# Kernel tuning notes

Measured on AMD Instinct MI355X. Metric: run time of the kernel, lower is better.

## Reference

```python
import jax, jax.numpy as jnp
import numpy as np

N_HEADS = 8
PROJ_DIM = 32


def _phi(x):
    # elu(x) + 1 feature map (always > 0)
    return jax.nn.elu(x) + 1.0


def _causal_linear(pq, pk, v):
    # Faithful to torch _linear_kernelized_attention masked branch:
    #   dpq_l = pq_l - pq_{l-1} (with pq_{-1}=0)
    #   result_l = cumsum_{m<=l} (dpq_m . v_m) * pk_m
    # The torch code materializes (N,H,L,D,D); here the identical math is
    # computed via a per-position scalar c_m = dpq_m . v_m, O(L*D) memory.
    dpq = pq - jnp.concatenate([jnp.zeros_like(pq[..., :1, :]), pq[..., :-1, :]], axis=-2)
    c = jnp.einsum('nhld,nhld->nhl', dpq, v)[..., None]  # (N,H,L,1)
    return jnp.cumsum(c * pk, axis=-2)  # (N,H,L,D)


def _bidir_linear(pq, pk, v):
    # Non-masked linear path: (pk^T v) first, then pq @ (.)
    right = jnp.einsum('nhld,nhle->nhde', pk, v)
    return jnp.einsum('nhqd,nhde->nhqe', pq, right)


def _attention(Y, X, Wq, Wk, Wv, mask):
    N, Lq, Dm = Y.shape
    Lk = X.shape[1]
    H, Pd = N_HEADS, PROJ_DIM
    # torch Linear: x @ W^T
    q = (Y @ Wq.T).reshape(N, Lq, H, Pd).transpose(0, 2, 1, 3)  # (N,H,Lq,Pd)
    k = (X @ Wk.T).reshape(N, Lk, H, Pd).transpose(0, 2, 1, 3)
    v = (X @ Wv.T).reshape(N, Lk, H, Pd).transpose(0, 2, 1, 3)
    pq, pk = _phi(q), _phi(k)
    fn = _causal_linear if mask else _bidir_linear
    num = fn(pq, pk, v)
    den = fn(pq, pk, jnp.ones_like(v))  # v_scale = ones expanded to D
    A = num / den
    return A.transpose(0, 2, 1, 3).reshape(N, Lq, H * Pd)


def setup_inputs() -> dict:
    key = jax.random.key(0)
    kY, kX, kq, kk, kv = jax.random.split(key, 5)
    N, L, dim = 2, 8192, N_HEADS * PROJ_DIM
    scale_in = 0.05            # keep phi(q),phi(k) ~ 1 so denominator stays positive
    scale_w = 1.0 / np.sqrt(dim)
    Y = scale_in * jax.random.normal(kY, (N, L, dim), dtype=jnp.float32)
    X = scale_in * jax.random.normal(kX, (N, L, dim), dtype=jnp.float32)
    Wq = scale_w * jax.random.normal(kq, (dim, dim), dtype=jnp.float32)
    Wk = scale_w * jax.random.normal(kk, (dim, dim), dtype=jnp.float32)
    Wv = scale_w * jax.random.normal(kv, (dim, dim), dtype=jnp.float32)
    return {"Y": Y, "X": X, "Wq": Wq, "Wk": Wk, "Wv": Wv, "mask": 1}


def reference(Y, X, Wq, Wk, Wv, mask):
    return _attention(Y, X, Wq, Wk, Wv, mask)
```

## Files before the change

kernel.cpp:

```cpp
#include <hip/hip_runtime.h>
#include <hip/hip_bf16.h>


typedef __attribute__((ext_vector_type(8))) short short8;
typedef __attribute__((ext_vector_type(4))) float f32x4;

__device__ __forceinline__ float phi_f(float x) {
    return x > 0.f ? x + 1.f : __expf(x);
}
__device__ __forceinline__ unsigned short f2bf(float x) {
    __hip_bfloat16 h = __float2bfloat16(x);
    return *reinterpret_cast<unsigned short*>(&h);
}
__device__ __forceinline__ float bf2f(unsigned short u) {
    return __uint_as_float(((unsigned int)u) << 16);
}

__global__ __launch_bounds__(256) void k_prepw(
        const float* __restrict__ Wq, const float* __restrict__ Wk,
        const float* __restrict__ Wv, unsigned short* __restrict__ Wf)
{
    const int g = blockIdx.x * 256 + threadIdx.x;
    const int mat = g >> 13, cc = g & 8191;
    const float* src = (mat == 0) ? Wq : (mat == 1 ? Wv : Wk);
    const int ln = cc & 15, qd = (cc >> 4) & 3, kt = (cc >> 6) & 7, jt = cc >> 9;
    const float* s = src + (size_t)(jt * 16 + ln) * 256 + kt * 32 + qd * 8;
    f32x4 f0 = __builtin_nontemporal_load((const f32x4*)s);
    f32x4 f1 = __builtin_nontemporal_load((const f32x4*)(s + 4));
    short8 o;
    o[0] = f2bf(f0[0]); o[1] = f2bf(f0[1]); o[2] = f2bf(f0[2]); o[3] = f2bf(f0[3]);
    o[4] = f2bf(f1[0]); o[5] = f2bf(f1[1]); o[6] = f2bf(f1[2]); o[7] = f2bf(f1[3]);
    *(short8*)(Wf + (size_t)g * 8) = o;
}

#define LDA 280

__global__ __launch_bounds__(512, 4) void k_gemm(
        const float* __restrict__ Y, const float* __restrict__ X,
        const unsigned short* __restrict__ Wf,
        unsigned short* __restrict__ pk_out,
        float* __restrict__ c_out, float* __restrict__ cd_out,
        float* __restrict__ tot)
{
    __shared__ __align__(16) unsigned short Ys[33 * LDA];
    __shared__ __align__(16) unsigned short Xs[32 * LDA];
    __shared__ float scc[32][8], scd[32][8];
    __shared__ __align__(16) unsigned short spk[32 * 264];

    const int rb = blockIdx.x;
    const int n = rb >> 8, tile = rb & 255;
    const int mbase = rb * 32, lseg0 = tile * 32;
    const bool hasprev = (tile != 0);
    const int t = threadIdx.x, w = t >> 6, lane = t & 63;
    const int ln = lane & 15, qd = lane >> 4;

#pragma unroll
    for (int it = 0; it < 8; ++it) {
        const int idx = t + it * 512;
        const int half = idx >> 11, row = (idx >> 6) & 31, c4 = idx & 63;
        const float* s = (half ? X : Y) + (size_t)(mbase + row) * 256 + c4 * 4;
        f32x4 f = __builtin_nontemporal_load((const f32x4*)s);
        ushort4 h4;
        h4.x = f2bf(f[0]); h4.y = f2bf(f[1]); h4.z = f2bf(f[2]); h4.w = f2bf(f[3]);
        unsigned short* dst = half ? Xs : Ys;
        *(ushort4*)&dst[row * LDA + c4 * 4] = h4;
    }
    if (t < 64) {
        const int prow = hasprev ? mbase - 1 : mbase;
        f32x4 f = __builtin_nontemporal_load((const f32x4*)(Y + (size_t)prow * 256 + t * 4));
        ushort4 h4;
        h4.x = f2bf(f[0]); h4.y = f2bf(f[1]); h4.z = f2bf(f[2]); h4.w = f2bf(f[3]);
        *(ushort4*)&Ys[32 * LDA + t * 4] = h4;
    }
    __syncthreads();

    f32x4 aq[2][2], av[2][2], akk[2][2], aqp[2];
#pragma unroll
    for (int i = 0; i < 2; ++i)
#pragma unroll
        for (int j = 0; j < 2; ++j) {
            aq[i][j]  = (f32x4){0.f, 0.f, 0.f, 0.f};
            av[i][j]  = (f32x4){0.f, 0.f, 0.f, 0.f};
            akk[i][j] = (f32x4){0.f, 0.f, 0.f, 0.f};
        }
    aqp[0] = (f32x4){0.f, 0.f, 0.f, 0.f};
    aqp[1] = (f32x4){0.f, 0.f, 0.f, 0.f};
    const short8 z8 = {0, 0, 0, 0, 0, 0, 0, 0};
    const short8* W8 = (const short8*)Wf;

#pragma unroll
    for (int kt = 0; kt < 8; ++kt) {
        const int ko = kt * 32 + qd * 8;
        short8 ay0 = *(const short8*)&Ys[ln * LDA + ko];
        short8 ay1 = *(const short8*)&Ys[(16 + ln) * LDA + ko];
        short8 ax0 = *(const short8*)&Xs[ln * LDA + ko];
        short8 ax1 = *(const short8*)&Xs[(16 + ln) * LDA + ko];
        short8 ext = *(const short8*)&Ys[32 * LDA + ko];
        short8 ayp = (ln == 15) ? ext : z8;
#pragma unroll
        for (int jj = 0; jj < 2; ++jj) {
            const int jt = w * 2 + jj;
            short8 bq = W8[(((0 * 16 + jt) * 8 + kt) << 6) + lane];
            short8 bv = W8[(((1 * 16 + jt) * 8 + kt) << 6) + lane];
            short8 bk = W8[(((2 * 16 + jt) * 8 + kt) << 6) + lane];
            aq[0][jj]  = __builtin_amdgcn_mfma_f32_16x16x32_bf16(ay0, bq, aq[0][jj], 0, 0, 0);
            aq[1][jj]  = __builtin_amdgcn_mfma_f32_16x16x32_bf16(ay1, bq, aq[1][jj], 0, 0, 0);
            aqp[jj]    = __builtin_amdgcn_mfma_f32_16x16x32_bf16(ayp, bq, aqp[jj], 0, 0, 0);
            av[0][jj]  = __builtin_amdgcn_mfma_f32_16x16x32_bf16(ax0, bv, av[0][jj], 0, 0, 0);
            av[1][jj]  = __builtin_amdgcn_mfma_f32_16x16x32_bf16(ax1, bv, av[1][jj], 0, 0, 0);
            akk[0][jj] = __builtin_amdgcn_mfma_f32_16x16x32_bf16(ax0, bk, akk[0][jj], 0, 0, 0);
            akk[1][jj] = __builtin_amdgcn_mfma_f32_16x16x32_bf16(ax1, bk, akk[1][jj], 0, 0, 0);
        }
    }

#pragma unroll
    for (int i = 0; i < 2; ++i)
#pragma unroll
        for (int jj = 0; jj < 2; ++jj)
#pragma unroll
            for (int r = 0; r < 4; ++r) aq[i][jj][r] = phi_f(aq[i][jj][r]);
    float pprev[2];
#pragma unroll
    for (int jj = 0; jj < 2; ++jj) {
        float p15 = __shfl(aqp[jj][3], 48 + ln);
        pprev[jj] = hasprev ? phi_f(p15) : 0.f;
    }

    float cc_[2][4], cd_[2][4];
#pragma unroll
    for (int i = 0; i < 2; ++i)
#pragma unroll
        for (int r = 0; r < 4; ++r) { cc_[i][r] = 0.f; cd_[i][r] = 0.f; }
#pragma unroll
    for (int jj = 0; jj < 2; ++jj) {
        float carry = pprev[jj];
#pragma unroll
        for (int i = 0; i < 2; ++i) {
            const float p0 = aq[i][jj][0], p1 = aq[i][jj][1], p2 = aq[i][jj][2], p3 = aq[i][jj][3];
            const float up3 = __shfl_up(p3, 16);
            const float prev0 = (qd == 0) ? carry : up3;
            const float d0 = p0 - prev0, d1 = p1 - p0, d2 = p2 - p1, d3 = p3 - p2;
            cc_[i][0] += d0 * av[i][jj][0]; cd_[i][0] += d0;
            cc_[i][1] += d1 * av[i][jj][1]; cd_[i][1] += d1;
            cc_[i][2] += d2 * av[i][jj][2]; cd_[i][2] += d2;
            cc_[i][3] += d3 * av[i][jj][3]; cd_[i][3] += d3;
            carry = __shfl(p3, ln + 48);
        }
    }
#pragma unroll
    for (int i = 0; i < 2; ++i)
#pragma unroll
        for (int r = 0; r < 4; ++r) {
            float x = cc_[i][r];
            x += __shfl_xor(x, 1); x += __shfl_xor(x, 2);
            x += __shfl_xor(x, 4); x += __shfl_xor(x, 8);
            float y = cd_[i][r];
            y += __shfl_xor(y, 1); y += __shfl_xor(y, 2);
            y += __shfl_xor(y, 4); y += __shfl_xor(y, 8);
            if (ln == 0) {
                scc[i * 16 + qd * 4 + r][w] = x;
                scd[i * 16 + qd * 4 + r][w] = y;
            }
        }
    __syncthreads();
    {
        const int idx = t & 255, row = idx & 31, h = idx >> 5;
        const size_t gi = (size_t)(n * 8 + h) * 8192 + lseg0 + row;
        if (t < 256) __builtin_nontemporal_store(scc[row][h], &c_out[gi]);
        else         __builtin_nontemporal_store(scd[row][h], &cd_out[gi]);
    }

#pragma unroll
    for (int i = 0; i < 2; ++i)
#pragma unroll
        for (int jj = 0; jj < 2; ++jj)
#pragma unroll
            for (int r = 0; r < 4; ++r) akk[i][jj][r] = phi_f(akk[i][jj][r]);
#pragma unroll
    for (int jj = 0; jj < 2; ++jj) {
        float tn = 0.f, td = 0.f;
#pragma unroll
        for (int i = 0; i < 2; ++i)
#pragma unroll
            for (int r = 0; r < 4; ++r) {
                const int row = i * 16 + qd * 4 + r;
                const float pv = akk[i][jj][r];
                tn += scc[row][w] * pv;
                td += scd[row][w] * pv;
            }
        tn += __shfl_xor(tn, 16); tn += __shfl_xor(tn, 32);
        td += __shfl_xor(td, 16); td += __shfl_xor(td, 32);
        if (qd == 0) {
            const int d = jj * 16 + ln;
            const size_t bi = ((size_t)(n * 8 + w) * 256 + tile) * 64;
            __builtin_nontemporal_store(tn, &tot[bi + d]);
            __builtin_nontemporal_store(td, &tot[bi + 32 + d]);
        }
    }

#pragma unroll
    for (int i = 0; i < 2; ++i)
#pragma unroll
        for (int jj = 0; jj < 2; ++jj)
#pragma unroll
            for (int r = 0; r < 4; ++r)
                spk[(i * 16 + qd * 4 + r) * 264 + w * 32 + jj * 16 + ln] = f2bf(akk[i][jj][r]);
    __syncthreads();
#pragma unroll
    for (int it = 0; it < 2; ++it) {
        const int idx = t + 512 * it;
        const int row = idx >> 5, cg = idx & 31;
        short8 vals = *(const short8*)&spk[row * 264 + cg * 8];
        const int head = cg >> 2, d8 = (cg & 3) * 8;
        __builtin_nontemporal_store(
            vals, (short8*)(pk_out + ((size_t)(n * 8 + head) * 8192 + lseg0 + row) * 32 + d8));
    }
}

__global__ __launch_bounds__(256) void k_scan(
        const unsigned short* __restrict__ pk, const float* __restrict__ c,
        const float* __restrict__ cd, const float* __restrict__ tot,
        float* __restrict__ out)
{
    __shared__ __align__(16) unsigned short spk[128 * 32];
    __shared__ float sc[128], sd[128];
    __shared__ float wsum[4][64], stile[4][64];

    const int bx = blockIdx.x, seg = bx >> 6, blk = bx & 63;
    const int n = seg >> 3, h = seg & 7;
    const int t = threadIdx.x, l0 = blk * 128;
    const int wv = t >> 6, lane = t & 63;
    const int T = blk * 4;

    const float* tb = tot + (size_t)seg * 256 * 64 + lane;
    float p0 = 0.f, p1 = 0.f, p2 = 0.f, p3 = 0.f,
          p4 = 0.f, p5 = 0.f, p6 = 0.f, p7 = 0.f;
    int i = wv;
    for (; i + 28 < T; i += 32) {
        p0 += tb[(i)      * 64]; p1 += tb[(i + 4)  * 64];
        p2 += tb[(i + 8)  * 64]; p3 += tb[(i + 12) * 64];
        p4 += tb[(i + 16) * 64]; p5 += tb[(i + 20) * 64];
        p6 += tb[(i + 24) * 64]; p7 += tb[(i + 28) * 64];
    }
    for (; i < T; i += 4) p0 += tb[i * 64];
    wsum[wv][lane]  = ((p0 + p1) + (p2 + p3)) + ((p4 + p5) + (p6 + p7));
    stile[wv][lane] = tb[(T + wv) * 64];

#pragma unroll
    for (int it = 0; it < 2; ++it) {
        const int idx = t + 256 * it;
        short8 vv = __builtin_nontemporal_load(
            (const short8*)(pk + ((size_t)seg * 8192 + l0) * 32 + idx * 8));
        *(short8*)&spk[idx * 8] = vv;
    }
    if (t < 128) sc[t] = __builtin_nontemporal_load(&c[(size_t)seg * 8192 + l0 + t]);
    else         sd[t - 128] = __builtin_nontemporal_load(&cd[(size_t)seg * 8192 + l0 + (t - 128)]);
    __syncthreads();

    if (t < 128) {
        const int g = t >> 5, d = t & 31;
        float rn  = (wsum[0][d] + wsum[1][d]) + (wsum[2][d] + wsum[3][d]);
        float rd_ = (wsum[0][32 + d] + wsum[1][32 + d]) + (wsum[2][32 + d] + wsum[3][32 + d]);
#pragma unroll
        for (int i2 = 0; i2 < 3; ++i2)
            if (i2 < g) { rn += stile[i2][d]; rd_ += stile[i2][32 + d]; }
        float* ob = out + ((size_t)n * 8192 + l0 + g * 32) * 256 + h * 32 + d;
#pragma unroll
        for (int p = 0; p < 32; ++p) {
            const int m = g * 32 + p;
            const float pkv = bf2f(spk[m * 32 + d]);
            rn  += sc[m] * pkv;
            rd_ += sd[m] * pkv;
            __builtin_nontemporal_store(rn / rd_, &ob[(size_t)p * 256]);
        }
    }
}

extern "C" void kernel_launch(void* const* d_in, const int* in_sizes, int n_in,
                              void* d_out, int out_size, void* d_ws, size_t ws_size,
                              hipStream_t stream)
{
    const float* Y  = (const float*)d_in[0];
    const float* X  = (const float*)d_in[1];
    const float* Wq = (const float*)d_in[2];
    const float* Wk = (const float*)d_in[3];
    const float* Wv = (const float*)d_in[4];
    float* out = (float*)d_out;

    float* ws = (float*)d_ws;
    unsigned short* Wf = (unsigned short*)ws;
    unsigned short* pk = (unsigned short*)(ws + 98304);
    float* c   = ws + 98304 + 2097152;
    float* cd  = c  + 131072;
    float* tot = cd + 131072;

    hipLaunchKernelGGL(k_prepw, dim3(96),   dim3(256), 0, stream, Wq, Wk, Wv, Wf);
    hipLaunchKernelGGL(k_gemm,  dim3(512),  dim3(512), 0, stream,
                       Y, X, Wf, pk, c, cd, tot);
    hipLaunchKernelGGL(k_scan,  dim3(1024), dim3(256), 0, stream, pk, c, cd, tot, out);
}
```

Measured before the change: 116.0 us.

## Process 64-row tiles per GEMM block with prefetched weight fragments and cached stores

Each k_gemm block now handles two 32-row tiles (64 rows), so every weight fragment loaded from global memory feeds twice as many MFMAs. The grid is halved to 256 blocks. The weight fragments are prefetched two k-steps ahead through a three-slot register ring. Nontemporal stores and loads for the pk, c, cd and tot intermediates become ordinary ones, so the scan kernel can hit them in cache. In exchange, register and LDS use roughly double and occupancy drops to 2 blocks per CU. With only 256 blocks, the GPU may also be underfilled.

```diff
diff --git a/kernel.cpp b/kernel.cpp
--- a/kernel.cpp
+++ b/kernel.cpp
@@ -35,29 +35,30 @@
 
 #define LDA 280
 
-__global__ __launch_bounds__(512, 4) void k_gemm(
+__global__ __launch_bounds__(512, 2) void k_gemm(
         const float* __restrict__ Y, const float* __restrict__ X,
         const unsigned short* __restrict__ Wf,
         unsigned short* __restrict__ pk_out,
         float* __restrict__ c_out, float* __restrict__ cd_out,
         float* __restrict__ tot)
 {
-    __shared__ __align__(16) unsigned short Ys[33 * LDA];
-    __shared__ __align__(16) unsigned short Xs[32 * LDA];
-    __shared__ float scc[32][8], scd[32][8];
-    __shared__ __align__(16) unsigned short spk[32 * 264];
+    __shared__ __align__(16) unsigned short Ys[65 * LDA];
+    __shared__ __align__(16) unsigned short Xs[64 * LDA];
+    __shared__ float scc[64][8], scd[64][8];
+    __shared__ __align__(16) unsigned short spk[64 * 264];
 
     const int rb = blockIdx.x;
-    const int n = rb >> 8, tile = rb & 255;
-    const int mbase = rb * 32, lseg0 = tile * 32;
-    const bool hasprev = (tile != 0);
+    const int n = rb >> 7, tpair = rb & 127;
+    const int mbase = rb * 64;
+    const int tile0 = tpair * 2, lseg0 = tpair * 64;
+    const bool hasprev = (tpair != 0);
     const int t = threadIdx.x, w = t >> 6, lane = t & 63;
     const int ln = lane & 15, qd = lane >> 4;
 
 #pragma unroll
-    for (int it = 0; it < 8; ++it) {
+    for (int it = 0; it < 16; ++it) {
         const int idx = t + it * 512;
-        const int half = idx >> 11, row = (idx >> 6) & 31, c4 = idx & 63;
+        const int half = idx >> 12, row = (idx >> 6) & 63, c4 = idx & 63;
         const float* s = (half ? X : Y) + (size_t)(mbase + row) * 256 + c4 * 4;
         f32x4 f = __builtin_nontemporal_load((const f32x4*)s);
         ushort4 h4;
@@ -70,55 +71,83 @@
         f32x4 f = __builtin_nontemporal_load((const f32x4*)(Y + (size_t)prow * 256 + t * 4));
         ushort4 h4;
         h4.x = f2bf(f[0]); h4.y = f2bf(f[1]); h4.z = f2bf(f[2]); h4.w = f2bf(f[3]);
-        *(ushort4*)&Ys[32 * LDA + t * 4] = h4;
+        *(ushort4*)&Ys[64 * LDA + t * 4] = h4;
     }
     __syncthreads();
 
-    f32x4 aq[2][2], av[2][2], akk[2][2], aqp[2];
-#pragma unroll
-    for (int i = 0; i < 2; ++i)
-#pragma unroll
-        for (int j = 0; j < 2; ++j) {
-            aq[i][j]  = (f32x4){0.f, 0.f, 0.f, 0.f};
-            av[i][j]  = (f32x4){0.f, 0.f, 0.f, 0.f};
-            akk[i][j] = (f32x4){0.f, 0.f, 0.f, 0.f};
-        }
+    f32x4 aq[2][2][2], av[2][2][2], akk[2][2][2], aqp[2];
+#pragma unroll
+    for (int t2 = 0; t2 < 2; ++t2)
+#pragma unroll
+        for (int i = 0; i < 2; ++i)
+#pragma unroll
+            for (int j = 0; j < 2; ++j) {
+                aq[t2][i][j]  = (f32x4){0.f, 0.f, 0.f, 0.f};
+                av[t2][i][j]  = (f32x4){0.f, 0.f, 0.f, 0.f};
+                akk[t2][i][j] = (f32x4){0.f, 0.f, 0.f, 0.f};
+            }
     aqp[0] = (f32x4){0.f, 0.f, 0.f, 0.f};
     aqp[1] = (f32x4){0.f, 0.f, 0.f, 0.f};
     const short8 z8 = {0, 0, 0, 0, 0, 0, 0, 0};
     const short8* W8 = (const short8*)Wf;
+    const int jt0 = 2 * w;
+
+    short8 Bq[3][2], Bv[3][2], Bk[3][2];
+#define LOADB(slot, kt_)                                                   \
+    {                                                                      \
+        _Pragma("unroll")                                                  \
+        for (int jj = 0; jj < 2; ++jj) {                                   \
+            const int jt = jt0 + jj;                                       \
+            Bq[slot][jj] = W8[(((0 * 16 + jt) * 8 + (kt_)) << 6) + lane];  \
+            Bv[slot][jj] = W8[(((1 * 16 + jt) * 8 + (kt_)) << 6) + lane];  \
+            Bk[slot][jj] = W8[(((2 * 16 + jt) * 8 + (kt_)) << 6) + lane];  \
+        }                                                                  \
+    }
+    LOADB(0, 0);
+    LOADB(1, 1);
 
 #pragma unroll
     for (int kt = 0; kt < 8; ++kt) {
+        if (kt + 2 < 8) LOADB((kt + 2) % 3, kt + 2);
         const int ko = kt * 32 + qd * 8;
-        short8 ay0 = *(const short8*)&Ys[ln * LDA + ko];
-        short8 ay1 = *(const short8*)&Ys[(16 + ln) * LDA + ko];
-        short8 ax0 = *(const short8*)&Xs[ln * LDA + ko];
-        short8 ax1 = *(const short8*)&Xs[(16 + ln) * LDA + ko];
-        short8 ext = *(const short8*)&Ys[32 * LDA + ko];
+        short8 ay[2][2], ax[2][2];
+#pragma unroll
+        for (int t2 = 0; t2 < 2; ++t2)
+#pragma unroll
+            for (int i = 0; i < 2; ++i) {
+                ay[t2][i] = *(const short8*)&Ys[(t2 * 32 + i * 16 + ln) * LDA + ko];
+                ax[t2][i] = *(const short8*)&Xs[(t2 * 32 + i * 16 + ln) * LDA + ko];
+            }
+        short8 ext = *(const short8*)&Ys[64 * LDA + ko];
         short8 ayp = (ln == 15) ? ext : z8;
+        const int sl = kt % 3;
 #pragma unroll
         for (int jj = 0; jj < 2; ++jj) {
-            const int jt = w * 2 + jj;
-            short8 bq = W8[(((0 * 16 + jt) * 8 + kt) << 6) + lane];
-            short8 bv = W8[(((1 * 16 + jt) * 8 + kt) << 6) + lane];
-            short8 bk = W8[(((2 * 16 + jt) * 8 + kt) << 6) + lane];
-            aq[0][jj]  = __builtin_amdgcn_mfma_f32_16x16x32_bf16(ay0, bq, aq[0][jj], 0, 0, 0);
-            aq[1][jj]  = __builtin_amdgcn_mfma_f32_16x16x32_bf16(ay1, bq, aq[1][jj], 0, 0, 0);
-            aqp[jj]    = __builtin_amdgcn_mfma_f32_16x16x32_bf16(ayp, bq, aqp[jj], 0, 0, 0);
-            av[0][jj]  = __builtin_amdgcn_mfma_f32_16x16x32_bf16(ax0, bv, av[0][jj], 0, 0, 0);
-            av[1][jj]  = __builtin_amdgcn_mfma_f32_16x16x32_bf16(ax1, bv, av[1][jj], 0, 0, 0);
-            akk[0][jj] = __builtin_amdgcn_mfma_f32_16x16x32_bf16(ax0, bk, akk[0][jj], 0, 0, 0);
-            akk[1][jj] = __builtin_amdgcn_mfma_f32_16x16x32_bf16(ax1, bk, akk[1][jj], 0, 0, 0);
+            aq[0][0][jj] = __builtin_amdgcn_mfma_f32_16x16x32_bf16(ay[0][0], Bq[sl][jj], aq[0][0][jj], 0, 0, 0);
+            aq[0][1][jj] = __builtin_amdgcn_mfma_f32_16x16x32_bf16(ay[0][1], Bq[sl][jj], aq[0][1][jj], 0, 0, 0);
+            aq[1][0][jj] = __builtin_amdgcn_mfma_f32_16x16x32_bf16(ay[1][0], Bq[sl][jj], aq[1][0][jj], 0, 0, 0);
+            aq[1][1][jj] = __builtin_amdgcn_mfma_f32_16x16x32_bf16(ay[1][1], Bq[sl][jj], aq[1][1][jj], 0, 0, 0);
+            aqp[jj]      = __builtin_amdgcn_mfma_f32_16x16x32_bf16(ayp,      Bq[sl][jj], aqp[jj],      0, 0, 0);
+            av[0][0][jj] = __builtin_amdgcn_mfma_f32_16x16x32_bf16(ax[0][0], Bv[sl][jj], av[0][0][jj], 0, 0, 0);
+            av[0][1][jj] = __builtin_amdgcn_mfma_f32_16x16x32_bf16(ax[0][1], Bv[sl][jj], av[0][1][jj], 0, 0, 0);
+            av[1][0][jj] = __builtin_amdgcn_mfma_f32_16x16x32_bf16(ax[1][0], Bv[sl][jj], av[1][0][jj], 0, 0, 0);
+            av[1][1][jj] = __builtin_amdgcn_mfma_f32_16x16x32_bf16(ax[1][1], Bv[sl][jj], av[1][1][jj], 0, 0, 0);
+            akk[0][0][jj] = __builtin_amdgcn_mfma_f32_16x16x32_bf16(ax[0][0], Bk[sl][jj], akk[0][0][jj], 0, 0, 0);
+            akk[0][1][jj] = __builtin_amdgcn_mfma_f32_16x16x32_bf16(ax[0][1], Bk[sl][jj], akk[0][1][jj], 0, 0, 0);
+            akk[1][0][jj] = __builtin_amdgcn_mfma_f32_16x16x32_bf16(ax[1][0], Bk[sl][jj], akk[1][0][jj], 0, 0, 0);
+            akk[1][1][jj] = __builtin_amdgcn_mfma_f32_16x16x32_bf16(ax[1][1], Bk[sl][jj], akk[1][1][jj], 0, 0, 0);
         }
     }
-
-#pragma unroll
-    for (int i = 0; i < 2; ++i)
-#pragma unroll
-        for (int jj = 0; jj < 2; ++jj)
-#pragma unroll
-            for (int r = 0; r < 4; ++r) aq[i][jj][r] = phi_f(aq[i][jj][r]);
+#undef LOADB
+
+#pragma unroll
+    for (int t2 = 0; t2 < 2; ++t2)
+#pragma unroll
+        for (int i = 0; i < 2; ++i)
+#pragma unroll
+            for (int jj = 0; jj < 2; ++jj)
+#pragma unroll
+                for (int r = 0; r < 4; ++r) aq[t2][i][jj][r] = phi_f(aq[t2][i][jj][r]);
     float pprev[2];
 #pragma unroll
     for (int jj = 0; jj < 2; ++jj) {
@@ -126,94 +155,107 @@
         pprev[jj] = hasprev ? phi_f(p15) : 0.f;
     }
 
-    float cc_[2][4], cd_[2][4];
-#pragma unroll
-    for (int i = 0; i < 2; ++i)
-#pragma unroll
-        for (int r = 0; r < 4; ++r) { cc_[i][r] = 0.f; cd_[i][r] = 0.f; }
+    float cc_[2][2][4], cd_[2][2][4];
+#pragma unroll
+    for (int t2 = 0; t2 < 2; ++t2)
+#pragma unroll
+        for (int i = 0; i < 2; ++i)
+#pragma unroll
+            for (int r = 0; r < 4; ++r) { cc_[t2][i][r] = 0.f; cd_[t2][i][r] = 0.f; }
 #pragma unroll
     for (int jj = 0; jj < 2; ++jj) {
         float carry = pprev[jj];
 #pragma unroll
-        for (int i = 0; i < 2; ++i) {
-            const float p0 = aq[i][jj][0], p1 = aq[i][jj][1], p2 = aq[i][jj][2], p3 = aq[i][jj][3];
-            const float up3 = __shfl_up(p3, 16);
-            const float prev0 = (qd == 0) ? carry : up3;
-            const float d0 = p0 - prev0, d1 = p1 - p0, d2 = p2 - p1, d3 = p3 - p2;
-            cc_[i][0] += d0 * av[i][jj][0]; cd_[i][0] += d0;
-            cc_[i][1] += d1 * av[i][jj][1]; cd_[i][1] += d1;
-            cc_[i][2] += d2 * av[i][jj][2]; cd_[i][2] += d2;
-            cc_[i][3] += d3 * av[i][jj][3]; cd_[i][3] += d3;
-            carry = __shfl(p3, ln + 48);
-        }
-    }
-#pragma unroll
-    for (int i = 0; i < 2; ++i)
-#pragma unroll
-        for (int r = 0; r < 4; ++r) {
-            float x = cc_[i][r];
-            x += __shfl_xor(x, 1); x += __shfl_xor(x, 2);
-            x += __shfl_xor(x, 4); x += __shfl_xor(x, 8);
-            float y = cd_[i][r];
-            y += __shfl_xor(y, 1); y += __shfl_xor(y, 2);
-            y += __shfl_xor(y, 4); y += __shfl_xor(y, 8);
-            if (ln == 0) {
-                scc[i * 16 + qd * 4 + r][w] = x;
-                scd[i * 16 + qd * 4 + r][w] = y;
-            }
-        }
+        for (int t2 = 0; t2 < 2; ++t2)
+#pragma unroll
+            for (int i = 0; i < 2; ++i) {
+                const float p0 = aq[t2][i][jj][0], p1 = aq[t2][i][jj][1];
+                const float p2 = aq[t2][i][jj][2], p3 = aq[t2][i][jj][3];
+                const float up3 = __shfl_up(p3, 16);
+                const float prev0 = (qd == 0) ? carry : up3;
+                const float d0 = p0 - prev0, d1 = p1 - p0, d2 = p2 - p1, d3 = p3 - p2;
+                cc_[t2][i][0] += d0 * av[t2][i][jj][0]; cd_[t2][i][0] += d0;
+                cc_[t2][i][1] += d1 * av[t2][i][jj][1]; cd_[t2][i][1] += d1;
+                cc_[t2][i][2] += d2 * av[t2][i][jj][2]; cd_[t2][i][2] += d2;
+                cc_[t2][i][3] += d3 * av[t2][i][jj][3]; cd_[t2][i][3] += d3;
+                carry = __shfl(p3, ln + 48);
+            }
+    }
+#pragma unroll
+    for (int t2 = 0; t2 < 2; ++t2)
+#pragma unroll
+        for (int i = 0; i < 2; ++i)
+#pragma unroll
+            for (int r = 0; r < 4; ++r) {
+                float x = cc_[t2][i][r];
+                x += __shfl_xor(x, 1); x += __shfl_xor(x, 2);
+                x += __shfl_xor(x, 4); x += __shfl_xor(x, 8);
+                float y = cd_[t2][i][r];
+                y += __shfl_xor(y, 1); y += __shfl_xor(y, 2);
+                y += __shfl_xor(y, 4); y += __shfl_xor(y, 8);
+                if (ln == 0) {
+                    scc[t2 * 32 + i * 16 + qd * 4 + r][w] = x;
+                    scd[t2 * 32 + i * 16 + qd * 4 + r][w] = y;
+                }
+            }
     __syncthreads();
     {
-        const int idx = t & 255, row = idx & 31, h = idx >> 5;
+        const int row = t & 63, h = t >> 6;
         const size_t gi = (size_t)(n * 8 + h) * 8192 + lseg0 + row;
-        if (t < 256) __builtin_nontemporal_store(scc[row][h], &c_out[gi]);
-        else         __builtin_nontemporal_store(scd[row][h], &cd_out[gi]);
-    }
-
-#pragma unroll
-    for (int i = 0; i < 2; ++i)
-#pragma unroll
-        for (int jj = 0; jj < 2; ++jj)
-#pragma unroll
-            for (int r = 0; r < 4; ++r) akk[i][jj][r] = phi_f(akk[i][jj][r]);
-#pragma unroll
-    for (int jj = 0; jj < 2; ++jj) {
-        float tn = 0.f, td = 0.f;
-#pragma unroll
-        for (int i = 0; i < 2; ++i)
-#pragma unroll
-            for (int r = 0; r < 4; ++r) {
-                const int row = i * 16 + qd * 4 + r;
-                const float pv = akk[i][jj][r];
-                tn += scc[row][w] * pv;
-                td += scd[row][w] * pv;
-            }
-        tn += __shfl_xor(tn, 16); tn += __shfl_xor(tn, 32);
-        td += __shfl_xor(td, 16); td += __shfl_xor(td, 32);
-        if (qd == 0) {
-            const int d = jj * 16 + ln;
-            const size_t bi = ((size_t)(n * 8 + w) * 256 + tile) * 64;
-            __builtin_nontemporal_store(tn, &tot[bi + d]);
-            __builtin_nontemporal_store(td, &tot[bi + 32 + d]);
+        c_out[gi]  = scc[row][h];
+        cd_out[gi] = scd[row][h];
+    }
+
+#pragma unroll
+    for (int t2 = 0; t2 < 2; ++t2)
+#pragma unroll
+        for (int i = 0; i < 2; ++i)
+#pragma unroll
+            for (int jj = 0; jj < 2; ++jj)
+#pragma unroll
+                for (int r = 0; r < 4; ++r) akk[t2][i][jj][r] = phi_f(akk[t2][i][jj][r]);
+#pragma unroll
+    for (int t2 = 0; t2 < 2; ++t2)
+#pragma unroll
+        for (int jj = 0; jj < 2; ++jj) {
+            float tn = 0.f, td = 0.f;
+#pragma unroll
+            for (int i = 0; i < 2; ++i)
+#pragma unroll
+                for (int r = 0; r < 4; ++r) {
+                    const int row = t2 * 32 + i * 16 + qd * 4 + r;
+                    const float pv = akk[t2][i][jj][r];
+                    tn += scc[row][w] * pv;
+                    td += scd[row][w] * pv;
+                }
+            tn += __shfl_xor(tn, 16); tn += __shfl_xor(tn, 32);
+            td += __shfl_xor(td, 16); td += __shfl_xor(td, 32);
+            if (qd == 0) {
+                const int d = jj * 16 + ln;
+                const size_t bi = ((size_t)(n * 8 + w) * 256 + tile0 + t2) * 64;
+                tot[bi + d]      = tn;
+                tot[bi + 32 + d] = td;
+            }
         }
-    }
-
-#pragma unroll
-    for (int i = 0; i < 2; ++i)
-#pragma unroll
-        for (int jj = 0; jj < 2; ++jj)
-#pragma unroll
-            for (int r = 0; r < 4; ++r)
-                spk[(i * 16 + qd * 4 + r) * 264 + w * 32 + jj * 16 + ln] = f2bf(akk[i][jj][r]);
+
+#pragma unroll
+    for (int t2 = 0; t2 < 2; ++t2)
+#pragma unroll
+        for (int i = 0; i < 2; ++i)
+#pragma unroll
+            for (int jj = 0; jj < 2; ++jj)
+#pragma unroll
+                for (int r = 0; r < 4; ++r)
+                    spk[(t2 * 32 + i * 16 + qd * 4 + r) * 264 + w * 32 + jj * 16 + ln]
+                        = f2bf(akk[t2][i][jj][r]);
     __syncthreads();
 #pragma unroll
-    for (int it = 0; it < 2; ++it) {
+    for (int it = 0; it < 4; ++it) {
         const int idx = t + 512 * it;
         const int row = idx >> 5, cg = idx & 31;
         short8 vals = *(const short8*)&spk[row * 264 + cg * 8];
         const int head = cg >> 2, d8 = (cg & 3) * 8;
-        __builtin_nontemporal_store(
-            vals, (short8*)(pk_out + ((size_t)(n * 8 + head) * 8192 + lseg0 + row) * 32 + d8));
+        *(short8*)(pk_out + ((size_t)(n * 8 + head) * 8192 + lseg0 + row) * 32 + d8) = vals;
     }
 }
 
@@ -249,12 +291,10 @@
 #pragma unroll
     for (int it = 0; it < 2; ++it) {
         const int idx = t + 256 * it;
-        short8 vv = __builtin_nontemporal_load(
-            (const short8*)(pk + ((size_t)seg * 8192 + l0) * 32 + idx * 8));
-        *(short8*)&spk[idx * 8] = vv;
-    }
-    if (t < 128) sc[t] = __builtin_nontemporal_load(&c[(size_t)seg * 8192 + l0 + t]);
-    else         sd[t - 128] = __builtin_nontemporal_load(&cd[(size_t)seg * 8192 + l0 + (t - 128)]);
+        *(short8*)&spk[idx * 8] = *(const short8*)(pk + ((size_t)seg * 8192 + l0) * 32 + idx * 8);
+    }
+    if (t < 128) sc[t] = c[(size_t)seg * 8192 + l0 + t];
+    else         sd[t - 128] = cd[(size_t)seg * 8192 + l0 + (t - 128)];
     __syncthreads();
 
     if (t < 128) {
@@ -295,7 +335,7 @@
     float* tot = cd + 131072;
 
     hipLaunchKernelGGL(k_prepw, dim3(96),   dim3(256), 0, stream, Wq, Wk, Wv, Wf);
-    hipLaunchKernelGGL(k_gemm,  dim3(512),  dim3(512), 0, stream,
+    hipLaunchKernelGGL(k_gemm,  dim3(256),  dim3(512), 0, stream,
                        Y, X, Wf, pk, c, cd, tot);
     hipLaunchKernelGGL(k_scan,  dim3(1024), dim3(256), 0, stream, pk, c, cd, tot, out);
 }
```

Measured after the change: 113.7 us. -2.0%, faster.
